# Kernel tuning notes

Measured on AMD Instinct MI355X. Metric: run time of the kernel, lower is better.

Reference implementation:

```python
import jax, jax.numpy as jnp
import numpy as np

NEG = -9e15
ALPHA = 0.2  # LeakyReLU negative slope


def _gat_layer(x, W, a, mask):
    # x: [N, Fin], W: [Fin, Fout], a: [2*Fout, 1], mask: [N, N] bool
    h = x @ W                                  # [N, Fout]
    F = h.shape[1]
    # additive attention score: identical math to cat([h_i, h_j]) @ a
    f1 = h @ a[:F, 0]                          # [N]
    f2 = h @ a[F:, 0]                          # [N]
    e = jax.nn.leaky_relu(f1[:, None] + f2[None, :], ALPHA)  # [N, N]
    e = jnp.where(mask, e, NEG)
    attn = jax.nn.softmax(e, axis=1)           # dropout is identity in eval mode
    return attn @ h                            # [N, Fout]


def setup_inputs() -> dict:
    key = jax.random.key(0)
    ks = jax.random.split(key, 6)
    N, Fin, H, Fh, Fo = 4096, 256, 8, 64, 64
    features = jax.random.normal(ks[0], (N, Fin), dtype=jnp.float32)
    adj = jax.random.randint(ks[1], (N, N), 0, 2).astype(jnp.float32)
    W_heads = jax.random.normal(ks[2], (H, Fin, Fh), dtype=jnp.float32) * 0.1
    a_heads = jax.random.normal(ks[3], (H, 2 * Fh, 1), dtype=jnp.float32) * 0.1
    W_out = jax.random.normal(ks[4], (H * Fh, Fo), dtype=jnp.float32) * 0.1
    a_out = jax.random.normal(ks[5], (2 * Fo, 1), dtype=jnp.float32) * 0.1
    return {"features": features, "adj": adj, "W_heads": W_heads,
            "a_heads": a_heads, "W_out": W_out, "a_out": a_out}


def reference(features, adj, W_heads, a_heads, W_out, a_out):
    mask = adj > 0
    H = W_heads.shape[0]
    # loop over the small fixed set of heads (keeps peak memory at one NxN matrix)
    heads = [jax.nn.elu(_gat_layer(features, W_heads[i], a_heads[i], mask))
             for i in range(H)]
    x = jnp.concatenate(heads, axis=1)         # [N, H*Fh]
    return _gat_layer(x, W_out, a_out, mask)   # concat=False -> no elu
```

## Files before the change

### kernel.cpp

```cpp
#include <hip/hip_runtime.h>
#include <hip/hip_bf16.h>

#define N_NODES 4096
#define LOG2E 1.44269504088896340736f
#define JT 128

typedef __attribute__((ext_vector_type(8))) short bf16x8;
typedef __attribute__((ext_vector_type(4))) short bf16x4;
typedef __attribute__((ext_vector_type(4))) float f32x4;
typedef __attribute__((ext_vector_type(16))) float f32x16;

static __device__ __forceinline__ ushort f2bf(float x) {
    union { float f; unsigned u; } v; v.f = x;
    unsigned u = v.u;
    return (ushort)((u + 0x7FFFu + ((u >> 16) & 1u)) >> 16);
}

__global__ __launch_bounds__(256) void k_prologue(const float* __restrict__ adj,
        unsigned* __restrict__ maskw,
        const float* __restrict__ W1, ushort* __restrict__ Wh1, ushort* __restrict__ Wl1,
        const float* __restrict__ W2, ushort* __restrict__ Wh2, ushort* __restrict__ Wl2) {
    int b = blockIdx.x, t = threadIdx.x;
    if (b < 2048) {
        int idx = b * 256 + t;
        int row = idx >> 7, w = idx & 127;
        const float4* ap = (const float4*)(adj + (size_t)row * N_NODES + w * 32);
        unsigned bits = 0;
#pragma unroll
        for (int q = 0; q < 8; ++q) {
            float4 v = ap[q];
            bits |= (v.x > 0.f ? 1u : 0u) << (q * 4 + 0);
            bits |= (v.y > 0.f ? 1u : 0u) << (q * 4 + 1);
            bits |= (v.z > 0.f ? 1u : 0u) << (q * 4 + 2);
            bits |= (v.w > 0.f ? 1u : 0u) << (q * 4 + 3);
        }
        maskw[idx] = bits;
    } else {
        const float* W; ushort *Wh, *Wl; int idx, kshift;
        if (b < 2560) { W = W1; Wh = Wh1; Wl = Wl1; idx = (b - 2048) * 256 + t; kshift = 8; }
        else          { W = W2; Wh = Wh2; Wl = Wl2; idx = (b - 2560) * 256 + t; kshift = 9; }
        int K = 1 << kshift;
        int n = idx & 63;
        int k = (idx >> 6) & (K - 1);
        int h = idx >> (6 + kshift);
        float v = W[idx];
        ushort hi = f2bf(v);
        union { unsigned u; float f; } hv; hv.u = ((unsigned)hi) << 16;
        ushort lo = f2bf(v - hv.f);
        size_t dst = ((size_t)h * 64 + n) * K + k;
        Wh[dst] = hi; Wl[dst] = lo;
    }
}

__global__ __launch_bounds__(512) void k_gemm_h(const float* __restrict__ X,
        const ushort* __restrict__ Wh, const ushort* __restrict__ Wl,
        const float* __restrict__ a,
        ushort* __restrict__ Ht, float* __restrict__ Rc,
        float* __restrict__ Tc, ushort* __restrict__ G2b, int K) {
    int head = blockIdx.y;
    int t = threadIdx.x, wave = t >> 6, lane = t & 63;
    int c = lane & 15, g = lane >> 4;
    int i0 = blockIdx.x * 16;
    int kq = K >> 3;
    int kbeg = wave * kq;
    const float* xrow = X + (size_t)(i0 + c) * K;
    f32x4 acc[4] = {};
    for (int k0 = kbeg; k0 < kbeg + kq; k0 += 32) {
        const float4* xp = (const float4*)(xrow + k0 + g * 8);
        float4 xa = xp[0], xb = xp[1];
        float xs[8] = {xa.x, xa.y, xa.z, xa.w, xb.x, xb.y, xb.z, xb.w};
        union { ushort s[8]; bf16x8 v; } ah, al;
#pragma unroll
        for (int e = 0; e < 8; ++e) {
            ushort hb = f2bf(xs[e]);
            ah.s[e] = hb;
            union { unsigned u; float f; } hv; hv.u = ((unsigned)hb) << 16;
            al.s[e] = f2bf(xs[e] - hv.f);
        }
#pragma unroll
        for (int nt = 0; nt < 4; ++nt) {
            size_t boff = ((size_t)head * 64 + nt * 16 + c) * K + k0 + g * 8;
            bf16x8 bh = *(const bf16x8*)(Wh + boff);
            bf16x8 bl = *(const bf16x8*)(Wl + boff);
            acc[nt] = __builtin_amdgcn_mfma_f32_16x16x32_bf16(ah.v, bh, acc[nt], 0, 0, 0);
            acc[nt] = __builtin_amdgcn_mfma_f32_16x16x32_bf16(al.v, bh, acc[nt], 0, 0, 0);
            acc[nt] = __builtin_amdgcn_mfma_f32_16x16x32_bf16(ah.v, bl, acc[nt], 0, 0, 0);
        }
    }
    __shared__ float red[8][64][17];
#pragma unroll
    for (int nt = 0; nt < 4; ++nt)
#pragma unroll
        for (int r = 0; r < 4; ++r)
            red[wave][lane][nt * 4 + r] = acc[nt][r];
    __syncthreads();
    if (wave != 0) return;
#pragma unroll
    for (int nt = 0; nt < 4; ++nt)
#pragma unroll
        for (int r = 0; r < 4; ++r) {
            float s = 0.f;
#pragma unroll
            for (int w = 0; w < 8; ++w) s += red[w][lane][nt * 4 + r];
            acc[nt][r] = s;
        }
    float a1v[4], a2v[4];
#pragma unroll
    for (int nt = 0; nt < 4; ++nt) {
        a1v[nt] = a[head * 128 + nt * 16 + c];
        a2v[nt] = a[head * 128 + 64 + nt * 16 + c];
    }
    float G2f[4];
#pragma unroll
    for (int r = 0; r < 4; ++r) {
        float f1 = 0.f, f2 = 0.f;
#pragma unroll
        for (int nt = 0; nt < 4; ++nt) {
            f1 = __builtin_fmaf(acc[nt][r], a1v[nt], f1);
            f2 = __builtin_fmaf(acc[nt][r], a2v[nt], f2);
        }
#pragma unroll
        for (int o = 1; o < 16; o <<= 1) {
            f1 += __shfl_xor(f1, o);
            f2 += __shfl_xor(f2, o);
        }
        float g2 = __builtin_amdgcn_exp2f(0.2f * LOG2E * f2);
        G2f[r] = g2;
        if (c == 0) {
            int i = i0 + g * 4 + r;
            Rc [head * N_NODES + i] = __builtin_amdgcn_exp2f(-0.8f * LOG2E * f1);
            Tc [head * N_NODES + i] = __builtin_amdgcn_exp2f( 0.8f * LOG2E * f2);
            G2b[head * N_NODES + i] = f2bf(g2);
        }
    }
#pragma unroll
    for (int nt = 0; nt < 4; ++nt) {
        union { ushort s[4]; bf16x4 v; } pk;
#pragma unroll
        for (int r = 0; r < 4; ++r) pk.s[r] = f2bf(acc[nt][r] * G2f[r]);
        *(bf16x4*)(Ht + ((size_t)head * 64 + nt * 16 + c) * N_NODES + i0 + g * 4) = pk.v;
    }
}

__global__ __launch_bounds__(512) void k_gemm2(const float* __restrict__ accP,
        const float* __restrict__ Zp, int JS1,
        const ushort* __restrict__ Wh, const ushort* __restrict__ Wl,
        const float* __restrict__ a,
        ushort* __restrict__ Ht, float* __restrict__ Rc,
        float* __restrict__ Tc, ushort* __restrict__ G2b) {
    const int K = 512;
    int t = threadIdx.x, wave = t >> 6, lane = t & 63;
    int c = lane & 15, g = lane >> 4;
    int i0 = blockIdx.x * 16;
    int row = i0 + c;
    int hx = wave;
    float z = 0.f;
    for (int js = 0; js < JS1; ++js)
        z += Zp[(size_t)(hx * JS1 + js) * N_NODES + row];
    float rz = 1.0f / z;
    f32x4 acc[4] = {};
#pragma unroll
    for (int ki = 0; ki < 2; ++ki) {
        int k0 = wave * 64 + ki * 32;
        int n0 = ki * 32 + g * 8;
        float s[8] = {};
        for (int js = 0; js < JS1; ++js) {
            const float* apn = accP + ((size_t)(hx * JS1 + js) * N_NODES + row) * 64 + n0;
            float4 u0 = ((const float4*)apn)[0];
            float4 u1 = ((const float4*)apn)[1];
            s[0] += u0.x; s[1] += u0.y; s[2] += u0.z; s[3] += u0.w;
            s[4] += u1.x; s[5] += u1.y; s[6] += u1.z; s[7] += u1.w;
        }
        union { ushort sh[8]; bf16x8 v; } ah, al;
#pragma unroll
        for (int e = 0; e < 8; ++e) {
            float v = s[e] * rz;
            v = v > 0.f ? v : (__builtin_amdgcn_exp2f(v * LOG2E) - 1.f);
            ushort hb = f2bf(v);
            ah.sh[e] = hb;
            union { unsigned u; float f; } hv; hv.u = ((unsigned)hb) << 16;
            al.sh[e] = f2bf(v - hv.f);
        }
#pragma unroll
        for (int nt = 0; nt < 4; ++nt) {
            size_t boff = ((size_t)(nt * 16 + c)) * K + k0 + g * 8;
            bf16x8 bh = *(const bf16x8*)(Wh + boff);
            bf16x8 bl = *(const bf16x8*)(Wl + boff);
            acc[nt] = __builtin_amdgcn_mfma_f32_16x16x32_bf16(ah.v, bh, acc[nt], 0, 0, 0);
            acc[nt] = __builtin_amdgcn_mfma_f32_16x16x32_bf16(al.v, bh, acc[nt], 0, 0, 0);
            acc[nt] = __builtin_amdgcn_mfma_f32_16x16x32_bf16(ah.v, bl, acc[nt], 0, 0, 0);
        }
    }
    __shared__ float red[8][64][17];
#pragma unroll
    for (int nt = 0; nt < 4; ++nt)
#pragma unroll
        for (int r = 0; r < 4; ++r)
            red[wave][lane][nt * 4 + r] = acc[nt][r];
    __syncthreads();
    if (wave != 0) return;
#pragma unroll
    for (int nt = 0; nt < 4; ++nt)
#pragma unroll
        for (int r = 0; r < 4; ++r) {
            float s = 0.f;
#pragma unroll
            for (int w = 0; w < 8; ++w) s += red[w][lane][nt * 4 + r];
            acc[nt][r] = s;
        }
    float a1v[4], a2v[4];
#pragma unroll
    for (int nt = 0; nt < 4; ++nt) {
        a1v[nt] = a[nt * 16 + c];
        a2v[nt] = a[64 + nt * 16 + c];
    }
    float G2f[4];
#pragma unroll
    for (int r = 0; r < 4; ++r) {
        float f1 = 0.f, f2 = 0.f;
#pragma unroll
        for (int nt = 0; nt < 4; ++nt) {
            f1 = __builtin_fmaf(acc[nt][r], a1v[nt], f1);
            f2 = __builtin_fmaf(acc[nt][r], a2v[nt], f2);
        }
#pragma unroll
        for (int o = 1; o < 16; o <<= 1) {
            f1 += __shfl_xor(f1, o);
            f2 += __shfl_xor(f2, o);
        }
        float g2 = __builtin_amdgcn_exp2f(0.2f * LOG2E * f2);
        G2f[r] = g2;
        if (c == 0) {
            int i = i0 + g * 4 + r;
            Rc [i] = __builtin_amdgcn_exp2f(-0.8f * LOG2E * f1);
            Tc [i] = __builtin_amdgcn_exp2f( 0.8f * LOG2E * f2);
            G2b[i] = f2bf(g2);
        }
    }
#pragma unroll
    for (int nt = 0; nt < 4; ++nt) {
        union { ushort s[4]; bf16x4 v; } pk;
#pragma unroll
        for (int r = 0; r < 4; ++r) pk.s[r] = f2bf(acc[nt][r] * G2f[r]);
        *(bf16x4*)(Ht + ((size_t)(nt * 16 + c)) * N_NODES + i0 + g * 4) = pk.v;
    }
}

__global__ __launch_bounds__(256)
__attribute__((amdgpu_waves_per_eu(4, 4)))
void k_attn(const ushort* __restrict__ Ht,
        const float* __restrict__ Rc, const float* __restrict__ Tc,
        const ushort* __restrict__ G2b, const unsigned* __restrict__ maskw,
        float* __restrict__ accP, float* __restrict__ Zp, int JS) {
    int rb = blockIdx.x, js = blockIdx.y, head = blockIdx.z;
    int t = threadIdx.x, wave = t >> 6, lane = t & 63;
    int r32 = lane & 31, half = lane >> 5;
    int i0b = rb * 128;
    int i0w = i0b + wave * 32;
    int irow = i0w + r32;
    int jcount = N_NODES / JS;
    int j0 = js * jcount;
    int ntiles = jcount / JT;
    const float R = Rc[head * N_NODES + irow];

    __shared__ ushort Hs[2][64 * JT];
    __shared__ unsigned Ms[2][512];
    __shared__ float Ts[2][JT];
    __shared__ ushort G2s[2][JT];

    int nH = (wave * 4) * 4 + (lane >> 4);
    const ushort* gspH[4];
#pragma unroll
    for (int s = 0; s < 4; ++s) {
        int n = nH + s * 4;
        gspH[s] = Ht + ((size_t)head * 64 + n) * N_NODES + j0
                + (((lane & 15) ^ (n & 7)) << 3);
    }
    const unsigned* msrc[8];
#pragma unroll
    for (int s = 0; s < 8; ++s)
        msrc[s] = maskw + (size_t)(i0b + s * 16 + (lane >> 2)) * 128 + (j0 >> 5) + (lane & 3);
    const float*  tsrc = Tc  + (size_t)head * N_NODES + j0 + lane;
    const ushort* gsrc = G2b + (size_t)head * N_NODES + j0 + lane * 2;

    auto stage = [&](int b, int tile) {
        int go = tile * JT;
#pragma unroll
        for (int s = 0; s < 4; ++s)
            __builtin_amdgcn_global_load_lds((const unsigned*)(gspH[s] + go),
                    (unsigned*)&Hs[b][(wave * 4 + s) * 512], 16, 0, 0);
        if (wave == 0) {
#pragma unroll
            for (int s = 0; s < 8; ++s)
                __builtin_amdgcn_global_load_lds((const unsigned*)(msrc[s] + tile * 4),
                        (unsigned*)&Ms[b][s * 64], 4, 0, 0);
        } else if (wave == 1) {
#pragma unroll
            for (int s = 0; s < 2; ++s)
                __builtin_amdgcn_global_load_lds((const unsigned*)(tsrc + go + s * 64),
                        (unsigned*)&Ts[b][s * 64], 4, 0, 0);
        } else if (wave == 2) {
            __builtin_amdgcn_global_load_lds((const unsigned*)(gsrc + go),
                    (unsigned*)&G2s[b][0], 4, 0, 0);
        }
    };

    f32x16 acc0 = {}, acc1 = {}, acc2 = {};

    stage(0, 0);
    int buf = 0;
    for (int tile = 0; tile < ntiles; ++tile) {
        if (tile + 1 < ntiles) {
            stage(buf ^ 1, tile + 1);
            if (wave == 0)      asm volatile("s_waitcnt vmcnt(12)");
            else if (wave == 1) asm volatile("s_waitcnt vmcnt(6)");
            else if (wave == 2) asm volatile("s_waitcnt vmcnt(5)");
            else                asm volatile("s_waitcnt vmcnt(4)");
        } else {
            asm volatile("s_waitcnt vmcnt(0)");
        }
        __builtin_amdgcn_s_barrier();

        const char* hb = (const char*)&Hs[buf][0];
        union { uint4 v; unsigned w[4]; } mw;
        mw.v = *(const uint4*)&Ms[buf][(wave * 32 + r32) * 4];
#pragma unroll
        for (int itr = 0; itr < JT / 16; ++itr) {
            unsigned phys = (unsigned)(((itr * 2 + half) ^ (r32 & 7)) << 4);
            bf16x8 b0 = *(const bf16x8*)(hb + r32 * 256 + phys);
            bf16x8 b1 = *(const bf16x8*)(hb + (32 + r32) * 256 + phys);
            bf16x8 bg = *(const bf16x8*)(&G2s[buf][itr * 16 + half * 8]);
            unsigned mword = mw.w[itr >> 1];
            unsigned mshift = mword >> ((itr & 1) * 16 + half * 8);
            const float* tp = &Ts[buf][itr * 16 + half * 8];
            float4 ta = *(const float4*)tp;
            float4 tb = *(const float4*)(tp + 4);
            float tv[8] = {ta.x, ta.y, ta.z, ta.w, tb.x, tb.y, tb.z, tb.w};
            float p[8];
#pragma unroll
            for (int e = 0; e < 8; ++e) {
                int sm = (int)(mshift << (31 - e)) >> 31;
                float pe = fmaxf(tv[e], R);
                union { float f; int i; } pv; pv.f = pe;
                pv.i &= sm;
                p[e] = pv.f;
            }
            union { unsigned w[4]; bf16x8 v; } pa;
#pragma unroll
            for (int q = 0; q < 4; ++q)
                asm("v_cvt_pk_bf16_f32 %0, %1, %2"
                    : "=v"(pa.w[q]) : "v"(p[2 * q]), "v"(p[2 * q + 1]));
            acc0 = __builtin_amdgcn_mfma_f32_32x32x16_bf16(pa.v, b0, acc0, 0, 0, 0);
            acc1 = __builtin_amdgcn_mfma_f32_32x32x16_bf16(pa.v, b1, acc1, 0, 0, 0);
            acc2 = __builtin_amdgcn_mfma_f32_32x32x16_bf16(pa.v, bg, acc2, 0, 0, 0);
        }
        __builtin_amdgcn_s_barrier();
        buf ^= 1;
    }
    int slice = head * JS + js;
    if (r32 == 0) {
#pragma unroll
        for (int reg = 0; reg < 16; ++reg) {
            int drow = (reg & 3) + 8 * (reg >> 2) + 4 * half;
            Zp[(size_t)slice * N_NODES + i0w + drow] = acc2[reg];
        }
    }
    float* ap = accP + ((size_t)slice * N_NODES + i0w) * 64;
#pragma unroll
    for (int reg = 0; reg < 16; ++reg) {
        int drow = (reg & 3) + 8 * (reg >> 2) + 4 * half;
        ap[drow * 64 + r32] = acc0[reg];
        ap[drow * 64 + 32 + r32] = acc1[reg];
    }
}

__global__ __launch_bounds__(256) void k_combine2(const float* __restrict__ accP,
        const float* __restrict__ Zp, float* __restrict__ out, int JS) {
    int idx = blockIdx.x * 256 + threadIdx.x;
    int n = idx & 63, i = idx >> 6;
    float s = 0.f, z = 0.f;
    for (int j = 0; j < JS; ++j) {
        s += accP[((size_t)j * N_NODES + i) * 64 + n];
        z += Zp[(size_t)j * N_NODES + i];
    }
    out[idx] = s / z;
}

extern "C" void kernel_launch(void* const* d_in, const int* in_sizes, int n_in,
                              void* d_out, int out_size, void* d_ws, size_t ws_size,
                              hipStream_t stream) {
    const float* features = (const float*)d_in[0];
    const float* adj      = (const float*)d_in[1];
    const float* W_heads  = (const float*)d_in[2];
    const float* a_heads  = (const float*)d_in[3];
    const float* W_out    = (const float*)d_in[4];
    const float* a_out    = (const float*)d_in[5];
    float* out = (float*)d_out;

    int JS1, JS2;
    if (ws_size >= 43000000)      { JS1 = 4; JS2 = 32; }
    else if (ws_size >= 26000000) { JS1 = 2; JS2 = 16; }
    else                          { JS1 = 1; JS2 = 8;  }
    int slices = (8 * JS1 > JS2) ? 8 * JS1 : JS2;

    char* ws = (char*)d_ws;
    size_t off = 0;
    auto alloc = [&](size_t bytes) -> void* {
        void* p = ws + off; off = (off + bytes + 255) & ~(size_t)255; return p;
    };
    unsigned* maskw = (unsigned*)alloc((size_t)N_NODES * 128 * 4);
    ushort* Ht1 = (ushort*)alloc((size_t)8 * 64 * N_NODES * 2);
    ushort* Ht2 = (ushort*)alloc((size_t)64 * N_NODES * 2);
    float* Rc1  = (float*)alloc((size_t)8 * N_NODES * 4);
    float* Tc1  = (float*)alloc((size_t)8 * N_NODES * 4);
    ushort* G2b1 = (ushort*)alloc((size_t)8 * N_NODES * 2);
    float* Rc2  = (float*)alloc((size_t)N_NODES * 4);
    float* Tc2  = (float*)alloc((size_t)N_NODES * 4);
    ushort* G2b2 = (ushort*)alloc((size_t)N_NODES * 2);
    ushort* Wh1 = (ushort*)alloc((size_t)8 * 64 * 256 * 2);
    ushort* Wl1 = (ushort*)alloc((size_t)8 * 64 * 256 * 2);
    ushort* Wh2 = (ushort*)alloc((size_t)64 * 512 * 2);
    ushort* Wl2 = (ushort*)alloc((size_t)64 * 512 * 2);
    float* accP = (float*)alloc((size_t)slices * N_NODES * 64 * 4);
    float* Zp   = (float*)alloc((size_t)slices * N_NODES * 4);

    hipLaunchKernelGGL(k_prologue, dim3(2688), dim3(256), 0, stream,
                       adj, maskw, W_heads, Wh1, Wl1, W_out, Wh2, Wl2);
    hipLaunchKernelGGL(k_gemm_h, dim3(N_NODES / 16, 8), dim3(512), 0, stream,
                       features, Wh1, Wl1, a_heads, Ht1, Rc1, Tc1, G2b1, 256);
    hipLaunchKernelGGL(k_attn, dim3(32, JS1, 8), dim3(256), 0, stream,
                       Ht1, Rc1, Tc1, G2b1, maskw, accP, Zp, JS1);
    hipLaunchKernelGGL(k_gemm2, dim3(N_NODES / 16), dim3(512), 0, stream,
                       accP, Zp, JS1, Wh2, Wl2, a_out, Ht2, Rc2, Tc2, G2b2);
    hipLaunchKernelGGL(k_attn, dim3(32, JS2, 1), dim3(256), 0, stream,
                       Ht2, Rc2, Tc2, G2b2, maskw, accP, Zp, JS2);
    hipLaunchKernelGGL(k_combine2, dim3(N_NODES * 64 / 256), dim3(256), 0, stream,
                       accP, Zp, out, JS2);
}
```

Measured before the change: 121.6 us.

## Balance staging loads across waves and rotate tile order per block

The mask-word loads into LDS are now spread across all four waves, two rows each, instead of wave 0 issuing eight. The T and G2 loads go to waves 1-3, so every wave issues a similar number of async loads and the vmcnt waits are evened out. Each block also starts its j-tile walk at a rotated offset derived from block, split and head indices, so concurrent blocks are less likely to hit the same Ht columns at the same time. The rotation assumes ntiles is a power of two, and the hand-written vmcnt counts must match the new per-wave load counts.

```diff
diff --git a/kernel.cpp b/kernel.cpp
--- a/kernel.cpp
+++ b/kernel.cpp
@@ -261,6 +261,8 @@
     int jcount = N_NODES / JS;
     int j0 = js * jcount;
     int ntiles = jcount / JT;
+    int ntm1 = ntiles - 1;
+    int rot = (rb + js * 3 + head * 5) & ntm1;
     const float R = Rc[head * N_NODES + irow];
 
     __shared__ ushort Hs[2][64 * JT];
@@ -276,12 +278,12 @@
         gspH[s] = Ht + ((size_t)head * 64 + n) * N_NODES + j0
                 + (((lane & 15) ^ (n & 7)) << 3);
     }
-    const unsigned* msrc[8];
-#pragma unroll
-    for (int s = 0; s < 8; ++s)
-        msrc[s] = maskw + (size_t)(i0b + s * 16 + (lane >> 2)) * 128 + (j0 >> 5) + (lane & 3);
-    const float*  tsrc = Tc  + (size_t)head * N_NODES + j0 + lane;
-    const ushort* gsrc = G2b + (size_t)head * N_NODES + j0 + lane * 2;
+    const unsigned* msA = maskw + (size_t)(i0b + (2 * wave) * 16 + (lane >> 2)) * 128
+                        + (j0 >> 5) + (lane & 3);
+    const unsigned* msB = msA + (size_t)16 * 128;
+    const float*  tsrcA = Tc  + (size_t)head * N_NODES + j0 + lane;
+    const float*  tsrcB = Tc  + (size_t)head * N_NODES + j0 + 64 + lane;
+    const ushort* gsrc  = G2b + (size_t)head * N_NODES + j0 + lane * 2;
 
     auto stage = [&](int b, int tile) {
         int go = tile * JT;
@@ -289,33 +291,30 @@
         for (int s = 0; s < 4; ++s)
             __builtin_amdgcn_global_load_lds((const unsigned*)(gspH[s] + go),
                     (unsigned*)&Hs[b][(wave * 4 + s) * 512], 16, 0, 0);
-        if (wave == 0) {
-#pragma unroll
-            for (int s = 0; s < 8; ++s)
-                __builtin_amdgcn_global_load_lds((const unsigned*)(msrc[s] + tile * 4),
-                        (unsigned*)&Ms[b][s * 64], 4, 0, 0);
-        } else if (wave == 1) {
-#pragma unroll
-            for (int s = 0; s < 2; ++s)
-                __builtin_amdgcn_global_load_lds((const unsigned*)(tsrc + go + s * 64),
-                        (unsigned*)&Ts[b][s * 64], 4, 0, 0);
-        } else if (wave == 2) {
+        __builtin_amdgcn_global_load_lds(msA + tile * 4,
+                (unsigned*)&Ms[b][(2 * wave) * 64], 4, 0, 0);
+        __builtin_amdgcn_global_load_lds(msB + tile * 4,
+                (unsigned*)&Ms[b][(2 * wave + 1) * 64], 4, 0, 0);
+        if (wave == 1)
+            __builtin_amdgcn_global_load_lds((const unsigned*)(tsrcA + go),
+                    (unsigned*)&Ts[b][0], 4, 0, 0);
+        else if (wave == 2)
+            __builtin_amdgcn_global_load_lds((const unsigned*)(tsrcB + go),
+                    (unsigned*)&Ts[b][64], 4, 0, 0);
+        else if (wave == 3)
             __builtin_amdgcn_global_load_lds((const unsigned*)(gsrc + go),
                     (unsigned*)&G2s[b][0], 4, 0, 0);
-        }
     };
 
     f32x16 acc0 = {}, acc1 = {}, acc2 = {};
 
-    stage(0, 0);
+    stage(0, rot);
     int buf = 0;
-    for (int tile = 0; tile < ntiles; ++tile) {
-        if (tile + 1 < ntiles) {
-            stage(buf ^ 1, tile + 1);
-            if (wave == 0)      asm volatile("s_waitcnt vmcnt(12)");
-            else if (wave == 1) asm volatile("s_waitcnt vmcnt(6)");
-            else if (wave == 2) asm volatile("s_waitcnt vmcnt(5)");
-            else                asm volatile("s_waitcnt vmcnt(4)");
+    for (int tt = 0; tt < ntiles; ++tt) {
+        if (tt + 1 < ntiles) {
+            stage(buf ^ 1, (tt + 1 + rot) & ntm1);
+            if (wave == 0) asm volatile("s_waitcnt vmcnt(6)");
+            else           asm volatile("s_waitcnt vmcnt(7)");
         } else {
             asm volatile("s_waitcnt vmcnt(0)");
         }
```

After: 121.3 us. About the same (-0.3%).
